# Kernel optimization log

Hardware: AMD Instinct MI355X
Metric: run time of the kernel (lower is better)

Reference implementation:

```python
import jax, jax.numpy as jnp
import numpy as np

EPS = 1e-5

def _conv(x, w, b, dil, pad, groups):
    y = jax.lax.conv_general_dilated(
        x, w, window_strides=(1, 1), padding=[(pad, pad), (pad, pad)],
        rhs_dilation=(dil, dil), dimension_numbers=('NCHW', 'OIHW', 'NCHW'),
        feature_group_count=groups)
    return y + b[None, :, None, None]

def setup_inputs() -> dict:
    key = jax.random.key(0)
    ks = jax.random.split(key, 12)
    B, C, H, W = 16, 128, 128, 128
    half = C // 2  # 64
    x = jax.random.normal(ks[0], (B, C, H, W), dtype=jnp.float32)
    # depthwise 3x3 (groups=half) + pointwise 1x1
    dw_w = jax.random.normal(ks[1], (half, 1, 3, 3), dtype=jnp.float32) * 0.1
    dw_b = jax.random.normal(ks[2], (half,), dtype=jnp.float32) * 0.1
    pw_w = jax.random.normal(ks[3], (half, half, 1, 1), dtype=jnp.float32) * (1.0 / np.sqrt(half))
    pw_b = jax.random.normal(ks[4], (half,), dtype=jnp.float32) * 0.1
    # four 1->1 channel 3x3 convs with dilations 1..4 (weights shared across blocks)
    mcc_w = jax.random.normal(ks[5], (4, 1, 1, 3, 3), dtype=jnp.float32) * 0.2
    mcc_b = jax.random.normal(ks[6], (4,), dtype=jnp.float32) * 0.1
    gamma = jnp.ones((C,), dtype=jnp.float32)
    beta = jnp.zeros((C,), dtype=jnp.float32)
    return {"x": x, "dw_w": dw_w, "dw_b": dw_b, "pw_w": pw_w, "pw_b": pw_b,
            "mcc_w": mcc_w, "mcc_b": mcc_b, "gamma": gamma, "beta": beta}

def reference(x, dw_w, dw_b, pw_w, pw_b, mcc_w, mcc_b, gamma, beta):
    B, C, H, W = x.shape
    half = C // 2
    nblk = half // 4
    # split_channel: even channels -> x1, odd channels -> x2
    x1 = x[:, 0::2]
    x2 = x[:, 1::2]
    # branch 1: depthwise 3x3 then pointwise 1x1
    x1 = _conv(x1, dw_w, dw_b, dil=1, pad=1, groups=half)
    x1 = _conv(x1, pw_w, pw_b, dil=1, pad=0, groups=1)
    # branch 2: channel i of x2 goes through dilated conv (i mod 4); vectorize by
    # gathering channels j::4 and running one depthwise conv per dilation.
    ys = []
    for j in range(4):
        d = j + 1
        xj = x2[:, j::4]                       # [B, nblk, H, W]
        wj = jnp.tile(mcc_w[j], (nblk, 1, 1, 1))  # [nblk,1,3,3] shared kernel
        bj = jnp.tile(mcc_b[j], (nblk,))
        ys.append(_conv(xj, wj, bj, dil=d, pad=d, groups=nblk))
    # interleave back: channel 4*b+j <- ys[j][:, b]
    mcc = jnp.stack(ys, axis=2).reshape(B, half, H, W)
    fusion = jnp.concatenate([x1, mcc], axis=1)  # [B, C, H, W]
    # BatchNorm2d (training mode: batch statistics, biased variance) + ReLU
    mean = jnp.mean(fusion, axis=(0, 2, 3), keepdims=True)
    var = jnp.var(fusion, axis=(0, 2, 3), keepdims=True)
    norm = (fusion - mean) * jax.lax.rsqrt(var + EPS)
    out = norm * gamma[None, :, None, None] + beta[None, :, None, None]
    return jax.nn.relu(out)
```

## Files before the change

kernel.cpp:

```cpp
#include <hip/hip_runtime.h>
#include <hip/hip_bf16.h>

#define Bn 16
#define Cn 128
#define Hn 128
#define Wn 128
#define HWn (Hn*Wn)
#define CHWn (Cn*HWn)
#define HALF 64
#define NTOT (Bn*HWn)
#define NSLOT 32
#define NITEM 10240

#define DT_P 76
#define CB_P 136
#define SMEM_BYTES 22528

typedef __attribute__((ext_vector_type(8))) short short8;
typedef __attribute__((ext_vector_type(4))) float floatx4;
typedef float __attribute__((ext_vector_type(4))) f32x4;

__device__ __forceinline__ float4 fma4(float s, float4 v, float4 a) {
  a.x = fmaf(s, v.x, a.x); a.y = fmaf(s, v.y, a.y);
  a.z = fmaf(s, v.z, a.z); a.w = fmaf(s, v.w, a.w);
  return a;
}
__device__ __forceinline__ unsigned short f2bf(float f) {
  union { __hip_bfloat16 h; unsigned short u; } cv;
  cv.h = __float2bfloat16(f); return cv.u;
}
__device__ __forceinline__ float bf2f(unsigned short u) {
  union { unsigned short u; __hip_bfloat16 h; } cv; cv.u = u;
  return __bfloat162float(cv.h);
}
__device__ __forceinline__ unsigned pk2f(float a, float b) {
  return (unsigned)f2bf(a) | ((unsigned)f2bf(b) << 16);
}
__device__ __forceinline__ short8 ld_frag(const unsigned short* p) {
  union { uint2 u[2]; short8 s; } cv;
  cv.u[0] = *(const uint2*)p;
  cv.u[1] = *(const uint2*)(p + 4);
  return cv.s;
}
__device__ __forceinline__ void st_nt4(float* p, float4 v) {
  f32x4 w = {v.x, v.y, v.z, v.w};
  __builtin_nontemporal_store(w, (f32x4*)p);
}

__device__ __forceinline__ float4 row3(float4 acc, float4 B, float wa, float wb,
                                       float wc, int lane31) {
  float xl = __shfl_up(B.w, 1);
  float xr = __shfl_down(B.x, 1);
  if (lane31 == 0)  xl = 0.f;
  if (lane31 == 31) xr = 0.f;
  float4 L = make_float4(xl, B.x, B.y, B.z);
  float4 R = make_float4(B.y, B.z, B.w, xr);
  acc = fma4(wa, L, acc);
  acc = fma4(wb, B, acc);
  acc = fma4(wc, R, acc);
  return acc;
}

template<bool BF16>
__device__ __forceinline__ void dwpw_body(
    const int item, const int t, unsigned char* __restrict__ smem,
    const float* __restrict__ x, const float* __restrict__ pw_w,
    const float* __restrict__ dw_w, const float* __restrict__ dw_b,
    const float* __restrict__ pw_b, float* __restrict__ outf,
    __hip_bfloat16* __restrict__ outh, float* __restrict__ stats)
{
  unsigned short* DtCb = (unsigned short*)smem;
  float* dww  = (float*)(smem + 128*DT_P*2);
  float* sred = dww + 640;

  const int band = item & 7;
  const int ri   = item >> 3;
  const int h = band*16 + (ri & 15);
  const int b = ri >> 4;

  for (int i = t; i < 576; i += 256) {
    int k = i / 9, j = i - k*9;
    dww[j*64 + k] = dw_w[i];
  }
  if (t < 64)  dww[576 + t] = dw_b[t];
  if (t < 128) sred[t] = 0.f;
  __syncthreads();

  {
    const int lane31 = t & 31;
    const int px4 = lane31 << 2;
    const int k0 = t >> 5;
    const float* xb = x + (size_t)b*CHWn + (size_t)h*Wn + px4;
    const bool hasU = (h > 0), hasD = (h < Hn-1);
    const float4 z4 = make_float4(0.f,0.f,0.f,0.f);
    unsigned lo[4];
    #pragma unroll
    for (int i = 0; i < 8; ++i) {
      const int k = k0*8 + i;
      const float* xc = xb + (size_t)(2*k)*HWn;
      float4 r0 = hasU ? *(const float4*)(xc - Wn) : z4;
      float4 r1 = *(const float4*)xc;
      float4 r2 = hasD ? *(const float4*)(xc + Wn) : z4;
      float bk = dww[576 + k];
      float4 a = make_float4(bk, bk, bk, bk);
      a = row3(a, r0, dww[0*64+k], dww[1*64+k], dww[2*64+k], lane31);
      a = row3(a, r1, dww[3*64+k], dww[4*64+k], dww[5*64+k], lane31);
      a = row3(a, r2, dww[6*64+k], dww[7*64+k], dww[8*64+k], lane31);
      float av[4] = {a.x, a.y, a.z, a.w};
      if ((i & 1) == 0) {
        #pragma unroll
        for (int j = 0; j < 4; ++j) lo[j] = f2bf(av[j]);
      } else {
        #pragma unroll
        for (int j = 0; j < 4; ++j) {
          unsigned pk = lo[j] | ((unsigned)f2bf(av[j]) << 16);
          *(unsigned*)&DtCb[(px4+j)*DT_P + k0*8 + (i-1)] = pk;
        }
      }
    }
  }
  __syncthreads();

  const int lane = t & 63;
  const int wv   = t >> 6;
  const int q4   = lane >> 4;
  const int n16  = lane & 15;

  short8 Af[4][2], Bf[2][2];
  #pragma unroll
  for (int ct = 0; ct < 4; ++ct)
    #pragma unroll
    for (int kc = 0; kc < 2; ++kc) {
      const float* wp = pw_w + (ct*16 + n16)*64 + kc*32 + q4*8;
      float4 w0 = *(const float4*)wp;
      float4 w1 = *(const float4*)(wp + 4);
      union { unsigned u[4]; short8 s; } cv;
      cv.u[0] = pk2f(w0.x, w0.y); cv.u[1] = pk2f(w0.z, w0.w);
      cv.u[2] = pk2f(w1.x, w1.y); cv.u[3] = pk2f(w1.z, w1.w);
      Af[ct][kc] = cv.s;
    }
  #pragma unroll
  for (int nt = 0; nt < 2; ++nt)
    #pragma unroll
    for (int kc = 0; kc < 2; ++kc)
      Bf[nt][kc] = ld_frag(&DtCb[(wv*32 + nt*16 + n16)*DT_P + kc*32 + q4*8]);

  floatx4 C[4][2];
  #pragma unroll
  for (int ct = 0; ct < 4; ++ct) {
    float4 bs = *(const float4*)&pw_b[ct*16 + q4*4];
    floatx4 ini = {bs.x, bs.y, bs.z, bs.w};
    C[ct][0] = ini; C[ct][1] = ini;
  }
  #pragma unroll
  for (int kc = 0; kc < 2; ++kc)
    #pragma unroll
    for (int ct = 0; ct < 4; ++ct)
      #pragma unroll
      for (int nt = 0; nt < 2; ++nt)
        C[ct][nt] = __builtin_amdgcn_mfma_f32_16x16x32_bf16(
            Af[ct][kc], Bf[nt][kc], C[ct][nt], 0, 0, 0);

  __syncthreads();

  #pragma unroll
  for (int ct = 0; ct < 4; ++ct) {
    float S[4], Q[4];
    #pragma unroll
    for (int r = 0; r < 4; ++r) {
      float a = C[ct][0][r], c2 = C[ct][1][r];
      S[r] = a + c2;
      Q[r] = a*a + c2*c2;
    }
    #pragma unroll
    for (int off = 1; off < 16; off <<= 1)
      #pragma unroll
      for (int r = 0; r < 4; ++r) {
        S[r] += __shfl_xor(S[r], off);
        Q[r] += __shfl_xor(Q[r], off);
      }
    if (n16 == 0) {
      #pragma unroll
      for (int r = 0; r < 4; ++r) {
        int c = ct*16 + q4*4 + r;
        atomicAdd(&sred[c], S[r]);
        atomicAdd(&sred[64 + c], Q[r]);
      }
    }
  }

  const size_t ob = (size_t)b*CHWn + (size_t)h*Wn;
  if (BF16) {
    #pragma unroll
    for (int ct = 0; ct < 4; ++ct)
      #pragma unroll
      for (int nt = 0; nt < 2; ++nt)
        #pragma unroll
        for (int r = 0; r < 4; ++r) {
          int c  = ct*16 + q4*4 + r;
          int px = wv*32 + nt*16 + n16;
          DtCb[c*CB_P + px] = f2bf(C[ct][nt][r]);
        }
  } else {
    #pragma unroll
    for (int ct = 0; ct < 4; ++ct)
      #pragma unroll
      for (int nt = 0; nt < 2; ++nt)
        #pragma unroll
        for (int r = 0; r < 4; ++r) {
          int c  = ct*16 + q4*4 + r;
          int px = wv*32 + nt*16 + n16;
          outf[ob + (size_t)c*HWn + px] = C[ct][nt][r];
        }
  }
  __syncthreads();

  if (BF16) {
    for (int i = t; i < 1024; i += 256) {
      int c = i >> 4, p8 = (i & 15) << 3;
      uint4 v = *(const uint4*)&DtCb[c*CB_P + p8];
      *(uint4*)(outh + ob + (size_t)c*HWn + p8) = v;
    }
  }

  float* sg = stats + (item & (NSLOT-1))*256;
  if (t < 64)       atomicAdd(&sg[t], sred[t]);
  else if (t < 128) atomicAdd(&sg[64 + t], sred[t]);
}

template<int D> __device__ __forceinline__ float4 shiftL(float4 A, float4 B) {
  if (D == 1) return make_float4(A.w, B.x, B.y, B.z);
  if (D == 2) return make_float4(A.z, A.w, B.x, B.y);
  if (D == 3) return make_float4(A.y, A.z, A.w, B.x);
  return A;
}
template<int D> __device__ __forceinline__ float4 shiftR(float4 B, float4 C) {
  if (D == 1) return make_float4(B.y, B.z, B.w, C.x);
  if (D == 2) return make_float4(B.z, B.w, C.x, C.y);
  if (D == 3) return make_float4(B.w, C.x, C.y, C.z);
  return C;
}

template<bool BF16, int D>
__device__ __forceinline__ void mcc_compute(
    const float* __restrict__ xc, const float* __restrict__ wj, float bj,
    float* __restrict__ outf, __hip_bfloat16* __restrict__ outh,
    int t, int h0, float& s, float& q)
{
  const int px4 = (t & 31) << 2;
  const int rl  = t >> 5;
  const float4 z4 = make_float4(0.f,0.f,0.f,0.f);
  s = 0.f; q = 0.f;
  #pragma unroll
  for (int rr = 0; rr < 2; ++rr) {
    const int row = rl + rr*8;
    float4 acc = make_float4(bj, bj, bj, bj);
    #pragma unroll
    for (int dr = 0; dr < 3; ++dr) {
      const int gr = h0 + row + (dr-1)*D;
      float4 A4 = z4, B4 = z4, C4 = z4;
      if (gr >= 0 && gr < Hn) {
        const float* lrow = xc + (size_t)gr*Wn;
        B4 = *(const float4*)(lrow + px4);
        if (px4 > 0)   A4 = *(const float4*)(lrow + px4 - 4);
        if (px4 < 124) C4 = *(const float4*)(lrow + px4 + 4);
      }
      acc = fma4(wj[dr*3+0], shiftL<D>(A4, B4), acc);
      acc = fma4(wj[dr*3+1], B4, acc);
      acc = fma4(wj[dr*3+2], shiftR<D>(B4, C4), acc);
    }
    if (BF16) {
      uint2 pk; pk.x = pk2f(acc.x, acc.y); pk.y = pk2f(acc.z, acc.w);
      *(uint2*)(outh + (size_t)(h0+row)*Wn + px4) = pk;
    } else {
      *(float4*)(outf + (size_t)(h0+row)*Wn + px4) = acc;
    }
    s += acc.x + acc.y + acc.z + acc.w;
    q += acc.x*acc.x + acc.y*acc.y + acc.z*acc.z + acc.w*acc.w;
  }
}

template<bool BF16>
__device__ __forceinline__ void mcc_body(
    const int mi, const int t, unsigned char* __restrict__ smem,
    const float* __restrict__ x, const float* __restrict__ mcc_w,
    const float* __restrict__ mcc_b, float* __restrict__ outf,
    __hip_bfloat16* __restrict__ outh, float* __restrict__ stats)
{
  float* red = (float*)smem;

  const int hb = mi & 7;
  const int m  = (mi >> 3) & 63;
  const int b  = mi >> 9;
  const int j  = m & 3;
  const int h0 = hb << 4;

  const float* xc = x + (size_t)b*CHWn + (size_t)(2*m+1)*HWn;
  const size_t oo = (size_t)b*CHWn + (size_t)(HALF+m)*HWn;
  float* of = BF16 ? nullptr : outf + oo;
  __hip_bfloat16* oh = BF16 ? outh + oo : nullptr;
  const float* wj = mcc_w + j*9;
  const float bj = mcc_b[j];

  float s = 0.f, q = 0.f;
  switch (j) {
    case 0:  mcc_compute<BF16,1>(xc, wj, bj, of, oh, t, h0, s, q); break;
    case 1:  mcc_compute<BF16,2>(xc, wj, bj, of, oh, t, h0, s, q); break;
    case 2:  mcc_compute<BF16,3>(xc, wj, bj, of, oh, t, h0, s, q); break;
    default: mcc_compute<BF16,4>(xc, wj, bj, of, oh, t, h0, s, q); break;
  }

  #pragma unroll
  for (int off = 32; off > 0; off >>= 1) {
    s += __shfl_down(s, off);
    q += __shfl_down(q, off);
  }
  const int wvi = t >> 6;
  if ((t & 63) == 0) { red[wvi] = s; red[4+wvi] = q; }
  __syncthreads();
  if (t == 0) {
    float* sg = stats + (mi & (NSLOT-1))*256;
    atomicAdd(&sg[HALF + m],       red[0]+red[1]+red[2]+red[3]);
    atomicAdd(&sg[128 + HALF + m], red[4]+red[5]+red[6]+red[7]);
  }
}

template<bool BF16>
__global__ __launch_bounds__(256, 3) void fused_kernel(
    const float* __restrict__ x, const float* __restrict__ pw_w,
    const float* __restrict__ dw_w, const float* __restrict__ dw_b,
    const float* __restrict__ pw_b, const float* __restrict__ mcc_w,
    const float* __restrict__ mcc_b, float* __restrict__ outf,
    __hip_bfloat16* __restrict__ outh, float* __restrict__ stats)
{
  __shared__ __align__(16) unsigned char smem[SMEM_BYTES];
  const int bid = blockIdx.x;
  const int t = threadIdx.x;
  const int qt = bid / 5;
  if (bid - qt*5 == 0)
    dwpw_body<BF16>(qt, t, smem, x, pw_w, dw_w, dw_b, pw_b, outf, outh, stats);
  else
    mcc_body<BF16>(bid - qt - 1, t, smem, x, mcc_w, mcc_b, outf, outh, stats);
}

__global__ __launch_bounds__(256) void norm_bf_kernel(
    const unsigned short* __restrict__ inh, float* __restrict__ out,
    const float* __restrict__ statsr, const float* __restrict__ gamma,
    const float* __restrict__ beta)
{
  __shared__ float ssc[2];
  const int blk = blockIdx.x;
  const int plane = blk >> 2;
  const int quarter = blk & 3;
  const int c = plane & 127;
  const int t = threadIdx.x;

  const uint4* in = (const uint4*)(inh + (size_t)plane*HWn) + quarter*512;
  float* op = out + (size_t)plane*HWn + quarter*4096;
  uint4 p[2];
  #pragma unroll
  for (int i = 0; i < 2; ++i) p[i] = in[t + i*256];

  if (t < 64) {
    int idx = (t < 32) ? c : (128 + c);
    float v = statsr[(t & 31)*256 + idx];
    #pragma unroll
    for (int off = 1; off < 32; off <<= 1) v += __shfl_xor(v, off);
    float S = __shfl(v, 0);
    float Q = __shfl(v, 32);
    if (t == 0) {
      const float n = (float)NTOT;
      float mean = S / n;
      float var  = Q / n - mean*mean;
      float sc = gamma[c] / sqrtf(var + 1e-5f);
      ssc[0] = sc;
      ssc[1] = beta[c] - mean*sc;
    }
  }
  __syncthreads();
  const float sc = ssc[0], sh = ssc[1];

  #pragma unroll
  for (int i = 0; i < 2; ++i) {
    int idx = t + i*256;
    float4 a, bq;
    a.x = fmaxf(fmaf(bf2f(p[i].x & 0xffff), sc, sh), 0.f);
    a.y = fmaxf(fmaf(bf2f(p[i].x >> 16),    sc, sh), 0.f);
    a.z = fmaxf(fmaf(bf2f(p[i].y & 0xffff), sc, sh), 0.f);
    a.w = fmaxf(fmaf(bf2f(p[i].y >> 16),    sc, sh), 0.f);
    bq.x = fmaxf(fmaf(bf2f(p[i].z & 0xffff), sc, sh), 0.f);
    bq.y = fmaxf(fmaf(bf2f(p[i].z >> 16),    sc, sh), 0.f);
    bq.z = fmaxf(fmaf(bf2f(p[i].w & 0xffff), sc, sh), 0.f);
    bq.w = fmaxf(fmaf(bf2f(p[i].w >> 16),    sc, sh), 0.f);
    st_nt4(op + idx*8,     a);
    st_nt4(op + idx*8 + 4, bq);
  }
}

__global__ __launch_bounds__(256) void norm_f32_kernel(float* __restrict__ out,
    const float* __restrict__ statsr, const float* __restrict__ gamma,
    const float* __restrict__ beta)
{
  __shared__ float ssc[2];
  const int blk = blockIdx.x;
  const int plane = blk >> 2;
  const int quarter = blk & 3;
  const int c = plane & 127;
  const int t = threadIdx.x;

  if (t < 64) {
    int idx = (t < 32) ? c : (128 + c);
    float v = statsr[(t & 31)*256 + idx];
    #pragma unroll
    for (int off = 1; off < 32; off <<= 1) v += __shfl_xor(v, off);
    float S = __shfl(v, 0);
    float Q = __shfl(v, 32);
    if (t == 0) {
      const float n = (float)NTOT;
      float mean = S / n;
      float var  = Q / n - mean*mean;
      float sc = gamma[c] / sqrtf(var + 1e-5f);
      ssc[0] = sc;
      ssc[1] = beta[c] - mean*sc;
    }
  }
  __syncthreads();
  const float sc = ssc[0], sh = ssc[1];

  float* op = out + (size_t)plane*HWn + quarter*4096;
  #pragma unroll
  for (int i = 0; i < 4; ++i) {
    int idx = t + i*256;
    float4 v = ((const float4*)op)[idx];
    v.x = fmaxf(fmaf(v.x, sc, sh), 0.f);
    v.y = fmaxf(fmaf(v.y, sc, sh), 0.f);
    v.z = fmaxf(fmaf(v.z, sc, sh), 0.f);
    v.w = fmaxf(fmaf(v.w, sc, sh), 0.f);
    ((float4*)op)[idx] = v;
  }
}

extern "C" void kernel_launch(void* const* d_in, const int* in_sizes, int n_in,
                              void* d_out, int out_size, void* d_ws, size_t ws_size,
                              hipStream_t stream)
{
  (void)in_sizes; (void)n_in; (void)out_size;
  const float* x     = (const float*)d_in[0];
  const float* dw_w  = (const float*)d_in[1];
  const float* dw_b  = (const float*)d_in[2];
  const float* pw_w  = (const float*)d_in[3];
  const float* pw_b  = (const float*)d_in[4];
  const float* mcc_w = (const float*)d_in[5];
  const float* mcc_b = (const float*)d_in[6];
  const float* gamma = (const float*)d_in[7];
  const float* beta  = (const float*)d_in[8];
  float* out   = (float*)d_out;
  float* stats = (float*)d_ws;
  __hip_bfloat16* bf = (__hip_bfloat16*)((char*)d_ws + 34816);
  const size_t need = 34816 + (size_t)Bn*CHWn*2;
  const bool useBF = ws_size >= need;

  hipMemsetAsync(d_ws, 0, 32768, stream);
  if (useBF) {
    fused_kernel<true><<<NITEM, 256, 0, stream>>>(x, pw_w, dw_w, dw_b, pw_b,
                                                  mcc_w, mcc_b, nullptr, bf, stats);
    norm_bf_kernel<<<Bn*Cn*4, 256, 0, stream>>>((const unsigned short*)bf, out,
                                                stats, gamma, beta);
  } else {
    fused_kernel<false><<<NITEM, 256, 0, stream>>>(x, pw_w, dw_w, dw_b, pw_b,
                                                   mcc_w, mcc_b, out, nullptr, stats);
    norm_f32_kernel<<<Bn*Cn*4, 256, 0, stream>>>(out, stats, gamma, beta);
  }
}
```

Before: 333.0 us.

## Stage dilated-conv input rows in LDS and process whole planes per norm block

The dilated 3x3 branch now loads its 16+2D input rows into shared memory once per block (with zero-padded halo rows) and reads neighbours from LDS instead of issuing repeated global loads per tap row. Separately, the normalization kernels now handle a full plane per block instead of a quarter, cutting the block count by four and the per-block stats reduction overhead by the same factor. The LDS staging adds a barrier and needs up to 24x128 floats of shared memory, placed before the reduction scratch. Larger norm blocks hold more registers in flight and mean fewer blocks to hide latency.

```diff
diff --git a/kernel.cpp b/kernel.cpp
--- a/kernel.cpp
+++ b/kernel.cpp
@@ -245,11 +245,19 @@
 __device__ __forceinline__ void mcc_compute(
     const float* __restrict__ xc, const float* __restrict__ wj, float bj,
     float* __restrict__ outf, __hip_bfloat16* __restrict__ outh,
-    int t, int h0, float& s, float& q)
-{
+    float* lds, int t, int h0, float& s, float& q)
+{
+  const int R = 16 + 2*D;
+  for (int idx = t; idx < R*32; idx += 256) {
+    int r = idx >> 5, p4 = (idx & 31) << 2;
+    int gr = h0 - D + r;
+    float4 v = make_float4(0.f,0.f,0.f,0.f);
+    if (gr >= 0 && gr < Hn) v = *(const float4*)(xc + gr*Wn + p4);
+    *(float4*)&lds[r*128 + p4] = v;
+  }
+  __syncthreads();
   const int px4 = (t & 31) << 2;
   const int rl  = t >> 5;
-  const float4 z4 = make_float4(0.f,0.f,0.f,0.f);
   s = 0.f; q = 0.f;
   #pragma unroll
   for (int rr = 0; rr < 2; ++rr) {
@@ -257,14 +265,12 @@
     float4 acc = make_float4(bj, bj, bj, bj);
     #pragma unroll
     for (int dr = 0; dr < 3; ++dr) {
-      const int gr = h0 + row + (dr-1)*D;
-      float4 A4 = z4, B4 = z4, C4 = z4;
-      if (gr >= 0 && gr < Hn) {
-        const float* lrow = xc + (size_t)gr*Wn;
-        B4 = *(const float4*)(lrow + px4);
-        if (px4 > 0)   A4 = *(const float4*)(lrow + px4 - 4);
-        if (px4 < 124) C4 = *(const float4*)(lrow + px4 + 4);
-      }
+      const float* lrow = &lds[(row + dr*D)*128];
+      float4 B4 = *(const float4*)(lrow + px4);
+      float4 A4 = make_float4(0.f,0.f,0.f,0.f);
+      float4 C4 = make_float4(0.f,0.f,0.f,0.f);
+      if (px4 > 0)   A4 = *(const float4*)(lrow + px4 - 4);
+      if (px4 < 124) C4 = *(const float4*)(lrow + px4 + 4);
       acc = fma4(wj[dr*3+0], shiftL<D>(A4, B4), acc);
       acc = fma4(wj[dr*3+1], B4, acc);
       acc = fma4(wj[dr*3+2], shiftR<D>(B4, C4), acc);
@@ -287,7 +293,8 @@
     const float* __restrict__ mcc_b, float* __restrict__ outf,
     __hip_bfloat16* __restrict__ outh, float* __restrict__ stats)
 {
-  float* red = (float*)smem;
+  float* lds = (float*)smem;
+  float* red = lds + 24*128;
 
   const int hb = mi & 7;
   const int m  = (mi >> 3) & 63;
@@ -304,10 +311,10 @@
 
   float s = 0.f, q = 0.f;
   switch (j) {
-    case 0:  mcc_compute<BF16,1>(xc, wj, bj, of, oh, t, h0, s, q); break;
-    case 1:  mcc_compute<BF16,2>(xc, wj, bj, of, oh, t, h0, s, q); break;
-    case 2:  mcc_compute<BF16,3>(xc, wj, bj, of, oh, t, h0, s, q); break;
-    default: mcc_compute<BF16,4>(xc, wj, bj, of, oh, t, h0, s, q); break;
+    case 0:  mcc_compute<BF16,1>(xc, wj, bj, of, oh, lds, t, h0, s, q); break;
+    case 1:  mcc_compute<BF16,2>(xc, wj, bj, of, oh, lds, t, h0, s, q); break;
+    case 2:  mcc_compute<BF16,3>(xc, wj, bj, of, oh, lds, t, h0, s, q); break;
+    default: mcc_compute<BF16,4>(xc, wj, bj, of, oh, lds, t, h0, s, q); break;
   }
 
   #pragma unroll
@@ -349,17 +356,15 @@
     const float* __restrict__ beta)
 {
   __shared__ float ssc[2];
-  const int blk = blockIdx.x;
-  const int plane = blk >> 2;
-  const int quarter = blk & 3;
+  const int plane = blockIdx.x;
   const int c = plane & 127;
   const int t = threadIdx.x;
 
-  const uint4* in = (const uint4*)(inh + (size_t)plane*HWn) + quarter*512;
-  float* op = out + (size_t)plane*HWn + quarter*4096;
-  uint4 p[2];
-  #pragma unroll
-  for (int i = 0; i < 2; ++i) p[i] = in[t + i*256];
+  const uint4* in = (const uint4*)(inh + (size_t)plane*HWn);
+  float* op = out + (size_t)plane*HWn;
+  uint4 p[8];
+  #pragma unroll
+  for (int i = 0; i < 8; ++i) p[i] = in[t + i*256];
 
   if (t < 64) {
     int idx = (t < 32) ? c : (128 + c);
@@ -381,7 +386,7 @@
   const float sc = ssc[0], sh = ssc[1];
 
   #pragma unroll
-  for (int i = 0; i < 2; ++i) {
+  for (int i = 0; i < 8; ++i) {
     int idx = t + i*256;
     float4 a, bq;
     a.x = fmaxf(fmaf(bf2f(p[i].x & 0xffff), sc, sh), 0.f);
@@ -402,9 +407,7 @@
     const float* __restrict__ beta)
 {
   __shared__ float ssc[2];
-  const int blk = blockIdx.x;
-  const int plane = blk >> 2;
-  const int quarter = blk & 3;
+  const int plane = blockIdx.x;
   const int c = plane & 127;
   const int t = threadIdx.x;
 
@@ -427,9 +430,9 @@
   __syncthreads();
   const float sc = ssc[0], sh = ssc[1];
 
-  float* op = out + (size_t)plane*HWn + quarter*4096;
-  #pragma unroll
-  for (int i = 0; i < 4; ++i) {
+  float* op = out + (size_t)plane*HWn;
+  #pragma unroll
+  for (int i = 0; i < 16; ++i) {
     int idx = t + i*256;
     float4 v = ((const float4*)op)[idx];
     v.x = fmaxf(fmaf(v.x, sc, sh), 0.f);
@@ -464,11 +467,11 @@
   if (useBF) {
     fused_kernel<true><<<NITEM, 256, 0, stream>>>(x, pw_w, dw_w, dw_b, pw_b,
                                                   mcc_w, mcc_b, nullptr, bf, stats);
-    norm_bf_kernel<<<Bn*Cn*4, 256, 0, stream>>>((const unsigned short*)bf, out,
-                                                stats, gamma, beta);
+    norm_bf_kernel<<<Bn*Cn, 256, 0, stream>>>((const unsigned short*)bf, out,
+                                              stats, gamma, beta);
   } else {
     fused_kernel<false><<<NITEM, 256, 0, stream>>>(x, pw_w, dw_w, dw_b, pw_b,
                                                    mcc_w, mcc_b, out, nullptr, stats);
-    norm_f32_kernel<<<Bn*Cn*4, 256, 0, stream>>>(out, stats, gamma, beta);
-  }
-}
+    norm_f32_kernel<<<Bn*Cn, 256, 0, stream>>>(out, stats, gamma, beta);
+  }
+}
```

New measurement: 325.9 us. -2.1%, faster.
